# Optimization experiments

Hardware: AMD Instinct MI355X
Metric: run time of the kernel (lower is better)

The kernel has to match this reference:

```python
import jax, jax.numpy as jnp
import numpy as np

DIM = 2048
N_HEADS = 32
N_KV_HEADS = 8
HEAD_DIM = 64
REPEATS = N_HEADS // N_KV_HEADS
SLIDING_WINDOW = 1024
EPS = 1e-6
B, T = 2, 2048


def _alibi_slopes(n):
    # n_heads=32 is a power of 2
    r = 2.0 ** (-8.0 / n)
    return jnp.asarray([r ** i for i in range(n)], dtype=jnp.float32)


def _rms_norm(x, w, eps):
    # RMSNorm over the last (flattened heads*head_dim) axis
    var = jnp.mean(x * x, axis=-1, keepdims=True)
    return x * jax.lax.rsqrt(var + eps) * w


def setup_inputs() -> dict:
    key = jax.random.key(0)
    ks = jax.random.split(key, 6)
    s = 0.02
    return {
        "x": jax.random.normal(ks[0], (B, T, DIM), jnp.float32),
        "wq": jax.random.normal(ks[1], (N_HEADS * HEAD_DIM, DIM), jnp.float32) * s,
        "wk": jax.random.normal(ks[2], (N_KV_HEADS * HEAD_DIM, DIM), jnp.float32) * s,
        "wv": jax.random.normal(ks[3], (N_KV_HEADS * HEAD_DIM, DIM), jnp.float32) * s,
        "wo": jax.random.normal(ks[4], (DIM, N_HEADS * HEAD_DIM), jnp.float32) * s,
        "q_norm_w": jnp.ones((N_HEADS * HEAD_DIM,), jnp.float32),
        "k_norm_w": jnp.ones((N_KV_HEADS * HEAD_DIM,), jnp.float32),
    }


def reference(x, wq, wk, wv, wo, q_norm_w, k_norm_w):
    bsz, seqlen, _ = x.shape
    xq = _rms_norm(x @ wq.T, q_norm_w, EPS)
    xk = _rms_norm(x @ wk.T, k_norm_w, EPS)
    xv = x @ wv.T
    xq = xq.reshape(bsz, seqlen, N_HEADS, HEAD_DIM).transpose(0, 2, 1, 3)  # b h t d
    xk = xk.reshape(bsz, seqlen, N_KV_HEADS, HEAD_DIM).transpose(0, 2, 1, 3)
    xv = xv.reshape(bsz, seqlen, N_KV_HEADS, HEAD_DIM).transpose(0, 2, 1, 3)
    # GQA: repeat_interleave kv heads
    xk = jnp.repeat(xk, REPEATS, axis=1)
    xv = jnp.repeat(xv, REPEATS, axis=1)

    pos = jnp.arange(seqlen)
    dist = pos[None, :] - pos[:, None]                     # [t,s] = s - t (<=0 on causal side)
    slopes = _alibi_slopes(N_HEADS)
    alibi = slopes[:, None, None] * dist.astype(jnp.float32)  # [h,t,s]
    allowed = (dist <= 0) & (dist >= -SLIDING_WINDOW)      # causal + sliding window
    bias = jnp.where(allowed[None], alibi, -jnp.inf)       # [h,t,s]

    scale = 1.0 / jnp.sqrt(jnp.asarray(HEAD_DIM, jnp.float32))
    scores = jnp.einsum("bhtd,bhsd->bhts", xq, xk) * scale + bias[None]
    attn = jax.nn.softmax(scores, axis=-1)
    out = jnp.einsum("bhts,bhsd->bhtd", attn, xv)          # [b,h,t,d]
    out = out.transpose(0, 2, 1, 3).reshape(bsz, seqlen, N_HEADS * HEAD_DIM)
    return out @ wo.T
```

## Files before the change

kernel.cpp:

```cpp
#include <hip/hip_runtime.h>


typedef _Float16 f16;
typedef __attribute__((ext_vector_type(8))) _Float16 f16x8;
typedef __attribute__((ext_vector_type(4))) _Float16 f16x4;
typedef __attribute__((ext_vector_type(4))) float f32x4;

#define T_ 2048
#define NH 32
#define NKV 8
#define HD 64
#define WINDOW 1024
#define EPS_ 1e-6f
#define LOG2E 1.44269504088896340736f
#define LDQKV 3072

__device__ inline void async16(void* lds, const void* g) {
  __builtin_amdgcn_global_load_lds(
      (const __attribute__((address_space(1))) unsigned int*)g,
      (__attribute__((address_space(3))) unsigned int*)lds, 16, 0, 0);
}

struct CvtArgs {
  const float* src[5];
  f16* dst[5];
  int n4[5];
};
__global__ __launch_bounds__(256) void cvt_multi(CvtArgs a) {
  const int seg = blockIdx.y;
  const float* in = a.src[seg];
  f16* out = a.dst[seg];
  const int n4 = a.n4[seg];
  for (int i = blockIdx.x * blockDim.x + threadIdx.x; i < n4;
       i += gridDim.x * blockDim.x) {
    float4 v = ((const float4*)in)[i];
    f16x4 o;
    o[0] = (f16)v.x; o[1] = (f16)v.y; o[2] = (f16)v.z; o[3] = (f16)v.w;
    ((f16x4*)out)[i] = o;
  }
}

__global__ __launch_bounds__(256) void gemm_nt(const f16* __restrict__ A,
                                               const f16* __restrict__ B,
                                               void* __restrict__ C,
                                               int M, int N, int K, int ldc,
                                               int out_f32) {
  __shared__ f16 As[128 * 32];
  __shared__ f16 Bs[128 * 32];
  const int tid = threadIdx.x;
  const int lane = tid & 63, wave = tid >> 6;
  const int quad = (lane >> 4), l16 = lane & 15;
  const int wm = (wave >> 1) * 64, wn = (wave & 1) * 64;
  const int m0 = blockIdx.y * 128, n0 = blockIdx.x * 128;
  const int srow = tid >> 2, scol = (tid & 3) * 8;
  const f16* gA = A + (size_t)(m0 + srow) * K + scol;
  const f16* gB = B + (size_t)(n0 + srow) * K + scol;
  f16* lA = As + tid * 8;
  f16* lB = Bs + tid * 8;
  const size_t rowK64 = (size_t)64 * K;

  f32x4 acc[4][4] = {};

  for (int k0 = 0; k0 < K; k0 += 32) {
    async16(lA, gA + k0);
    async16(lA + 2048, gA + rowK64 + k0);
    async16(lB, gB + k0);
    async16(lB + 2048, gB + rowK64 + k0);
    __syncthreads();
    f16x8 af[4], bf[4];
#pragma unroll
    for (int i = 0; i < 4; ++i)
      af[i] = *(const f16x8*)(As + (wm + i * 16 + l16) * 32 + quad * 8);
#pragma unroll
    for (int i = 0; i < 4; ++i)
      bf[i] = *(const f16x8*)(Bs + (wn + i * 16 + l16) * 32 + quad * 8);
#pragma unroll
    for (int i = 0; i < 4; ++i)
#pragma unroll
      for (int j = 0; j < 4; ++j)
        acc[i][j] = __builtin_amdgcn_mfma_f32_16x16x32_f16(af[i], bf[j], acc[i][j], 0, 0, 0);
    __syncthreads();
  }
#pragma unroll
  for (int i = 0; i < 4; ++i) {
    const int row0 = m0 + wm + i * 16 + quad * 4;
#pragma unroll
    for (int j = 0; j < 4; ++j) {
      const int col = n0 + wn + j * 16 + l16;
#pragma unroll
      for (int r = 0; r < 4; ++r) {
        const float v = acc[i][j][r];
        if (out_f32) ((float*)C)[(size_t)(row0 + r) * ldc + col] = v;
        else         ((f16*)C)[(size_t)(row0 + r) * ldc + col] = (f16)v;
      }
    }
  }
}

__global__ __launch_bounds__(256) void rmsnorm2(f16* __restrict__ xqkv,
                                                const float* __restrict__ qw,
                                                const float* __restrict__ kw) {
  __shared__ float red[4];
  const int which = blockIdx.y;
  const int N = which ? 512 : 2048;
  const float* w = which ? kw : qw;
  f16* p = xqkv + (size_t)blockIdx.x * LDQKV + (which ? 2048 : 0);
  const int tid = threadIdx.x;
  const int per = N >> 8;
  float ss = 0.f;
#pragma unroll 4
  for (int i = 0; i < per; ++i) {
    const float v = (float)p[tid * per + i];
    ss += v * v;
  }
#pragma unroll
  for (int off = 32; off > 0; off >>= 1) ss += __shfl_down(ss, off);
  if ((tid & 63) == 0) red[tid >> 6] = ss;
  __syncthreads();
  const float scale = rsqrtf((red[0] + red[1] + red[2] + red[3]) / (float)N + EPS_);
#pragma unroll 4
  for (int i = 0; i < per; ++i) {
    const int c = tid * per + i;
    p[c] = (f16)((float)p[c] * scale * w[c]);
  }
}

__global__ __launch_bounds__(256) void vtrans(const f16* __restrict__ xqkv,
                                              f16* __restrict__ Vt) {
  __shared__ f16 L[64][72];
  const int t0 = blockIdx.x * 64;
  const int b = blockIdx.y >> 3, kh = blockIdx.y & 7;
  const int tid = threadIdx.x;
  const int r = tid >> 3, c = (tid & 7) * 8;
#pragma unroll
  for (int rp = 0; rp < 2; ++rp) {
    const int rr = r + rp * 32;
    *(f16x8*)(&L[rr][c]) =
        *(const f16x8*)(xqkv + (size_t)(b * T_ + t0 + rr) * LDQKV + 2560 + kh * 64 + c);
  }
  __syncthreads();
#pragma unroll
  for (int rp = 0; rp < 2; ++rp) {
    const int d = r + rp * 32;
    f16x8 o;
#pragma unroll
    for (int j = 0; j < 8; ++j) o[j] = L[c + j][d];
    *(f16x8*)(Vt + (size_t)((b * 8 + kh) * 64 + d) * T_ + t0 + c) = o;
  }
}

__global__ __launch_bounds__(256) void attn(const f16* __restrict__ Q,
                                            const f16* __restrict__ Kb,
                                            const f16* __restrict__ Vt_g,
                                            f16* __restrict__ O) {
  constexpr int LDW = 72;
  __shared__ f16 Qs[64 * LDW];
  __shared__ f16 Ks[64 * LDW];
  __shared__ f16 Vts[64 * LDW];
  __shared__ float Lx[4][16];

  const int qt = blockIdx.x, h = blockIdx.y, b = blockIdx.z;
  const int kh = h >> 2;
  const int q0 = qt * 64;
  const int tid = threadIdx.x;
  const int lane = tid & 63, wave = tid >> 6;
  const int quad = lane >> 4, l16 = lane & 15;
  const float scale2 = 0.125f * LOG2E;
  const float slope2 = exp2f(-0.25f * (float)h) * LOG2E;
  const float M2 = 10.0f;

  const int sr = tid >> 3, sc = (tid & 7) * 8;

#pragma unroll
  for (int rp = 0; rp < 2; ++rp) {
    const int rr = sr + rp * 32;
    *(f16x8*)(Qs + rr * LDW + sc) =
        *(const f16x8*)(Q + (size_t)(b * T_ + q0 + rr) * LDQKV + h * HD + sc);
  }
  __syncthreads();
  f16x8 qf[2];
#pragma unroll
  for (int kc = 0; kc < 2; ++kc)
    qf[kc] = *(const f16x8*)(Qs + (wave * 16 + l16) * LDW + kc * 32 + quad * 8);
  f16* Ps = Qs + wave * 16 * LDW;

  f32x4 o_acc[4] = {};
  float lsum = 0.f;

  const int kt_lo = (q0 >= WINDOW) ? ((q0 - WINDOW) >> 6) : 0;
  const int my_q = q0 + wave * 16 + l16;
  const size_t vbase = (size_t)((b * 8 + kh) * 64) * T_;

  float snbr[16];
#pragma unroll
  for (int nb = 0; nb < 4; ++nb)
#pragma unroll
    for (int r = 0; r < 4; ++r) snbr[nb * 4 + r] = slope2 * (float)(nb * 16 + r);
  float base = slope2 * (float)(kt_lo * 64 + quad * 4 - my_q) - M2;
  const float bstep = slope2 * 64.0f;

  f16x8 kreg[2], vreg[2];
  auto prefetch = [&](int k0) {
#pragma unroll
    for (int rp = 0; rp < 2; ++rp) {
      const int rr = sr + rp * 32;
      kreg[rp] = *(const f16x8*)(Kb + (size_t)(b * T_ + k0 + rr) * LDQKV + kh * HD + sc);
      vreg[rp] = *(const f16x8*)(Vt_g + vbase + (size_t)rr * T_ + k0 + sc);
    }
  };
  prefetch(kt_lo * 64);

  for (int kt = kt_lo; kt <= qt; ++kt) {
    const int k0 = kt * 64;
#pragma unroll
    for (int rp = 0; rp < 2; ++rp) {
      *(f16x8*)(Ks + (sr + rp * 32) * LDW + sc) = kreg[rp];
      *(f16x8*)(Vts + (sr + rp * 32) * LDW + sc) = vreg[rp];
    }
    __syncthreads();
    if (kt < qt) prefetch(k0 + 64);

    f32x4 s[4];
#pragma unroll
    for (int nb = 0; nb < 4; ++nb) {
      f32x4 a = {0.f, 0.f, 0.f, 0.f};
#pragma unroll
      for (int kc = 0; kc < 2; ++kc) {
        f16x8 kf = *(const f16x8*)(Ks + (nb * 16 + l16) * LDW + kc * 32 + quad * 8);
        a = __builtin_amdgcn_mfma_f32_16x16x32_f16(kf, qf[kc], a, 0, 0, 0);
      }
      s[nb] = a;
    }

    const bool maskt = (kt == qt) || (q0 + 63 - k0 > WINDOW);
#pragma unroll
    for (int nb = 0; nb < 4; ++nb) {
      f16x4 pk;
#pragma unroll
      for (int r = 0; r < 4; ++r) {
        float v = fmaf(s[nb][r], scale2, base + snbr[nb * 4 + r]);
        if (maskt) {
          const int dist = k0 + nb * 16 + quad * 4 + r - my_q;
          if (dist > 0 || dist < -WINDOW) v = -1e30f;
        }
        const float p = __builtin_amdgcn_exp2f(v);
        lsum += p;
        pk[r] = (f16)p;
      }
      *(f16x4*)(Ps + l16 * LDW + nb * 16 + quad * 4) = pk;
    }
    base += bstep;

#pragma unroll
    for (int nb = 0; nb < 4; ++nb) {
#pragma unroll
      for (int kc = 0; kc < 2; ++kc) {
        f16x8 pa = *(const f16x8*)(Ps + l16 * LDW + kc * 32 + quad * 8);
        f16x8 vb = *(const f16x8*)(Vts + (nb * 16 + l16) * LDW + kc * 32 + quad * 8);
        o_acc[nb] = __builtin_amdgcn_mfma_f32_16x16x32_f16(pa, vb, o_acc[nb], 0, 0, 0);
      }
    }
    __syncthreads();
  }

  lsum += __shfl_xor(lsum, 16);
  lsum += __shfl_xor(lsum, 32);
  if (quad == 0) Lx[wave][l16] = lsum;
  float rl[4];
#pragma unroll
  for (int r = 0; r < 4; ++r) rl[r] = 1.0f / Lx[wave][quad * 4 + r];

#pragma unroll
  for (int r = 0; r < 4; ++r) {
    const int q = q0 + wave * 16 + quad * 4 + r;
#pragma unroll
    for (int nb = 0; nb < 4; ++nb)
      O[(size_t)(b * T_ + q) * (NH * HD) + h * HD + nb * 16 + l16] =
          (f16)(o_acc[nb][r] * rl[r]);
  }
}

extern "C" void kernel_launch(void* const* d_in, const int* in_sizes, int n_in,
                              void* d_out, int out_size, void* d_ws, size_t ws_size,
                              hipStream_t stream) {
  const float* x  = (const float*)d_in[0];
  const float* wq = (const float*)d_in[1];
  const float* wk = (const float*)d_in[2];
  const float* wv = (const float*)d_in[3];
  const float* wo = (const float*)d_in[4];
  const float* qw = (const float*)d_in[5];
  const float* kw = (const float*)d_in[6];
  float* out = (float*)d_out;

  char* ws = (char*)d_ws;
  size_t off = 0;
  auto carve = [&](size_t bytes) -> char* {
    char* p = ws + off;
    off += (bytes + 255) & ~(size_t)255;
    return p;
  };
  f16* xh    = (f16*)carve((size_t)4096 * 2048 * 2);
  f16* wqkvh = (f16*)carve((size_t)3072 * 2048 * 2);
  f16* woh   = (f16*)carve((size_t)2048 * 2048 * 2);
  f16* xqkv  = (f16*)carve((size_t)4096 * 3072 * 2);
  f16* Vt = wqkvh + (size_t)2048 * 2048;
  f16* ao = xh;

  CvtArgs ca;
  ca.src[0] = x;  ca.dst[0] = xh;                            ca.n4[0] = (4096 * 2048) / 4;
  ca.src[1] = wq; ca.dst[1] = wqkvh;                         ca.n4[1] = (2048 * 2048) / 4;
  ca.src[2] = wk; ca.dst[2] = wqkvh + (size_t)2048 * 2048;   ca.n4[2] = (512 * 2048) / 4;
  ca.src[3] = wv; ca.dst[3] = wqkvh + (size_t)2560 * 2048;   ca.n4[3] = (512 * 2048) / 4;
  ca.src[4] = wo; ca.dst[4] = woh;                           ca.n4[4] = (2048 * 2048) / 4;
  cvt_multi<<<dim3(1024, 5), 256, 0, stream>>>(ca);

  gemm_nt<<<dim3(24, 32), 256, 0, stream>>>(xh, wqkvh, xqkv, 4096, 3072, 2048, LDQKV, 0);
  rmsnorm2<<<dim3(4096, 2), 256, 0, stream>>>(xqkv, qw, kw);
  vtrans<<<dim3(32, 16), 256, 0, stream>>>(xqkv, Vt);
  attn<<<dim3(32, 32, 2), 256, 0, stream>>>(xqkv, xqkv + 2048, Vt, ao);
  gemm_nt<<<dim3(16, 32), 256, 0, stream>>>(ao, woh, out, 4096, 2048, 2048, 2048, 1);
}
```

Before: 330.8 us.

## Replace GEMM with 256x256 double-buffered, swizzled-LDS 8-wave kernel

Replaces the 128x128, single-buffered, 4-wave GEMM with a 256x256 tile, 8-wave kernel. It uses K=64 steps, double-buffered LDS filled by async global-to-LDS loads, XOR-swizzled LDS addressing to avoid bank conflicts, and an XCD-aware block remap. Global loads for the next tile are interleaved with MFMA phases, and s_setprio raises priority during the MFMA phases. This is meant to raise arithmetic intensity and hide load latency in both projection GEMMs. In exchange it needs 128KB of dynamic LDS, which limits occupancy, and launches only 192 and 128 workgroups, which may underfill the GPU.

New measurement: 326.6 us. Within noise of the previous version (-1.3%).

```diff
diff --git a/kernel.cpp b/kernel.cpp
--- a/kernel.cpp
+++ b/kernel.cpp
@@ -40,56 +40,141 @@
   }
 }
 
-__global__ __launch_bounds__(256) void gemm_nt(const f16* __restrict__ A,
-                                               const f16* __restrict__ B,
-                                               void* __restrict__ C,
-                                               int M, int N, int K, int ldc,
-                                               int out_f32) {
-  __shared__ f16 As[128 * 32];
-  __shared__ f16 Bs[128 * 32];
+
+#define DSRD(p, off) (*(const f16x8*)((p) + (off)))
+
+#define LOADA(mh)                                                             \
+  {                                                                           \
+    _Pragma("unroll") for (int i = 0; i < 4; ++i) {                           \
+      af[i][0] = DSRD(cA, bufo + abase + (mh) * 8192 + i * 2048 + xk0);       \
+      af[i][1] = DSRD(cA, bufo + abase + (mh) * 8192 + i * 2048 + xk1);       \
+    }                                                                         \
+  }
+
+#define LOADB(bfv, nh)                                                        \
+  {                                                                           \
+    _Pragma("unroll") for (int j = 0; j < 2; ++j) {                           \
+      bfv[j][0] = DSRD(cB, bufo + bbase + (nh) * 4096 + j * 2048 + xk0);      \
+      bfv[j][1] = DSRD(cB, bufo + bbase + (nh) * 4096 + j * 2048 + xk1);      \
+    }                                                                         \
+  }
+
+#define FENCE_MFMA(mh, nh, bfv)                                               \
+  {                                                                           \
+    __builtin_amdgcn_s_barrier();                                             \
+    asm volatile("s_waitcnt lgkmcnt(0)" ::: "memory");                        \
+    __builtin_amdgcn_sched_barrier(0);                                        \
+    __builtin_amdgcn_s_setprio(1);                                            \
+    _Pragma("unroll") for (int i = 0; i < 4; ++i) {                           \
+      _Pragma("unroll") for (int j = 0; j < 2; ++j) {                         \
+        acc[(mh) * 4 + i][(nh) * 2 + j] =                                     \
+            __builtin_amdgcn_mfma_f32_16x16x32_f16(                           \
+                af[i][0], bfv[j][0], acc[(mh) * 4 + i][(nh) * 2 + j], 0, 0, 0); \
+        acc[(mh) * 4 + i][(nh) * 2 + j] =                                     \
+            __builtin_amdgcn_mfma_f32_16x16x32_f16(                           \
+                af[i][1], bfv[j][1], acc[(mh) * 4 + i][(nh) * 2 + j], 0, 0, 0); \
+      }                                                                       \
+    }                                                                         \
+    __builtin_amdgcn_s_setprio(0);                                            \
+  }
+
+__global__ __launch_bounds__(512, 2) void gemm_nt8(const f16* __restrict__ A,
+                                                   const f16* __restrict__ B,
+                                                   void* __restrict__ C,
+                                                   int M, int N, int K, int ldc,
+                                                   int out_f32) {
+  extern __shared__ char smem[];
+  f16* sA = (f16*)smem;
+  f16* sB = (f16*)(smem + 65536);
+
+  const int gx = gridDim.x;
+  const int nwg = gx * gridDim.y;
+  int bid = blockIdx.y * gx + blockIdx.x;
+  if (!(nwg & 7)) bid = (bid & 7) * (nwg >> 3) + (bid >> 3);
+  const int m0 = (bid / gx) * 256;
+  const int n0 = (bid % gx) * 256;
+
   const int tid = threadIdx.x;
-  const int lane = tid & 63, wave = tid >> 6;
-  const int quad = (lane >> 4), l16 = lane & 15;
-  const int wm = (wave >> 1) * 64, wn = (wave & 1) * 64;
-  const int m0 = blockIdx.y * 128, n0 = blockIdx.x * 128;
-  const int srow = tid >> 2, scol = (tid & 3) * 8;
-  const f16* gA = A + (size_t)(m0 + srow) * K + scol;
-  const f16* gB = B + (size_t)(n0 + srow) * K + scol;
-  f16* lA = As + tid * 8;
-  f16* lB = Bs + tid * 8;
-  const size_t rowK64 = (size_t)64 * K;
-
-  f32x4 acc[4][4] = {};
-
-  for (int k0 = 0; k0 < K; k0 += 32) {
-    async16(lA, gA + k0);
-    async16(lA + 2048, gA + rowK64 + k0);
-    async16(lB, gB + k0);
-    async16(lB + 2048, gB + rowK64 + k0);
-    __syncthreads();
-    f16x8 af[4], bf[4];
-#pragma unroll
-    for (int i = 0; i < 4; ++i)
-      af[i] = *(const f16x8*)(As + (wm + i * 16 + l16) * 32 + quad * 8);
-#pragma unroll
-    for (int i = 0; i < 4; ++i)
-      bf[i] = *(const f16x8*)(Bs + (wn + i * 16 + l16) * 32 + quad * 8);
-#pragma unroll
-    for (int i = 0; i < 4; ++i)
-#pragma unroll
-      for (int j = 0; j < 4; ++j)
-        acc[i][j] = __builtin_amdgcn_mfma_f32_16x16x32_f16(af[i], bf[j], acc[i][j], 0, 0, 0);
-    __syncthreads();
-  }
-#pragma unroll
-  for (int i = 0; i < 4; ++i) {
-    const int row0 = m0 + wm + i * 16 + quad * 4;
-#pragma unroll
-    for (int j = 0; j < 4; ++j) {
-      const int col = n0 + wn + j * 16 + l16;
+  const int lane = tid & 63;
+  const int wave = tid >> 6;
+  const int quad = lane >> 4, l16 = lane & 15;
+  const int wm = wave >> 2, wn = wave & 3;
+
+  const int srow = tid >> 3;
+  const int sgr = (((tid & 7) ^ (srow & 7))) * 8;
+  const f16* gA = A + (size_t)(m0 + srow) * K + sgr;
+  const f16* gB = B + (size_t)(n0 + srow) * K + sgr;
+  const size_t r64 = (size_t)64 * K;
+
+  const char* cA = (const char*)sA;
+  const char* cB = (const char*)sB;
+  const int xm = (l16 & 7) << 4;
+  const int xk0 = (quad * 16) ^ xm;
+  const int xk1 = (64 + quad * 16) ^ xm;
+  const int abase = (wm * 128 + l16) * 128;
+  const int bbase = (wn * 64 + l16) * 128;
+
+  f32x4 acc[8][4] = {};
+  const int nt = K >> 6;
+
+#pragma unroll
+  for (int a = 0; a < 4; ++a) {
+    async16(sA + a * 4096 + tid * 8, gA + (size_t)a * r64);
+    async16(sB + a * 4096 + tid * 8, gB + (size_t)a * r64);
+  }
+  asm volatile("s_waitcnt vmcnt(0)" ::: "memory");
+  __builtin_amdgcn_s_barrier();
+
+  for (int t = 0; t < nt; ++t) {
+    const int bufo = (t & 1) << 15;
+    f16* sAn = sA + ((t & 1) ^ 1) * 16384;
+    f16* sBn = sB + ((t & 1) ^ 1) * 16384;
+    const bool st = (t + 1 < nt);
+    const size_t gk = (size_t)(t + 1) * 64;
+
+    f16x8 af[4][2], bf0[2][2], bf1[2][2];
+
+    LOADA(0);
+    LOADB(bf0, 0);
+    if (st) {
+      async16(sAn + 0 * 4096 + tid * 8, gA + 0 * r64 + gk);
+      async16(sAn + 1 * 4096 + tid * 8, gA + 1 * r64 + gk);
+      async16(sBn + 0 * 4096 + tid * 8, gB + 0 * r64 + gk);
+      async16(sBn + 1 * 4096 + tid * 8, gB + 1 * r64 + gk);
+    }
+    FENCE_MFMA(0, 0, bf0);
+    __builtin_amdgcn_s_barrier();
+
+    LOADB(bf1, 1);
+    if (st) {
+      async16(sAn + 2 * 4096 + tid * 8, gA + 2 * r64 + gk);
+      async16(sAn + 3 * 4096 + tid * 8, gA + 3 * r64 + gk);
+      async16(sBn + 2 * 4096 + tid * 8, gB + 2 * r64 + gk);
+      async16(sBn + 3 * 4096 + tid * 8, gB + 3 * r64 + gk);
+    }
+    FENCE_MFMA(0, 1, bf1);
+    __builtin_amdgcn_s_barrier();
+
+    LOADA(1);
+    LOADB(bf0, 0);
+    FENCE_MFMA(1, 0, bf0);
+    __builtin_amdgcn_s_barrier();
+
+    LOADB(bf1, 1);
+    FENCE_MFMA(1, 1, bf1);
+    if (st) asm volatile("s_waitcnt vmcnt(0)" ::: "memory");
+    __builtin_amdgcn_s_barrier();
+  }
+
+#pragma unroll
+  for (int im = 0; im < 8; ++im) {
+    const int row0 = m0 + wm * 128 + im * 16 + quad * 4;
+#pragma unroll
+    for (int jn = 0; jn < 4; ++jn) {
+      const int col = n0 + wn * 64 + jn * 16 + l16;
 #pragma unroll
       for (int r = 0; r < 4; ++r) {
-        const float v = acc[i][j][r];
+        const float v = acc[im][jn][r];
         if (out_f32) ((float*)C)[(size_t)(row0 + r) * ldc + col] = v;
         else         ((f16*)C)[(size_t)(row0 + r) * ldc + col] = (f16)v;
       }
@@ -306,6 +391,14 @@
   f16* Vt = wqkvh + (size_t)2048 * 2048;
   f16* ao = xh;
 
+  static bool attr_done = false;
+  if (!attr_done) {
+    (void)hipFuncSetAttribute((const void*)gemm_nt8,
+                              hipFuncAttributeMaxDynamicSharedMemorySize,
+                              131072);
+    attr_done = true;
+  }
+
   CvtArgs ca;
   ca.src[0] = x;  ca.dst[0] = xh;                            ca.n4[0] = (4096 * 2048) / 4;
   ca.src[1] = wq; ca.dst[1] = wqkvh;                         ca.n4[1] = (2048 * 2048) / 4;
@@ -314,9 +407,9 @@
   ca.src[4] = wo; ca.dst[4] = woh;                           ca.n4[4] = (2048 * 2048) / 4;
   cvt_multi<<<dim3(1024, 5), 256, 0, stream>>>(ca);
 
-  gemm_nt<<<dim3(24, 32), 256, 0, stream>>>(xh, wqkvh, xqkv, 4096, 3072, 2048, LDQKV, 0);
+  gemm_nt8<<<dim3(12, 16), 512, 131072, stream>>>(xh, wqkvh, xqkv, 4096, 3072, 2048, LDQKV, 0);
   rmsnorm2<<<dim3(4096, 2), 256, 0, stream>>>(xqkv, qw, kw);
   vtrans<<<dim3(32, 16), 256, 0, stream>>>(xqkv, Vt);
   attn<<<dim3(32, 32, 2), 256, 0, stream>>>(xqkv, xqkv + 2048, Vt, ao);
-  gemm_nt<<<dim3(16, 32), 256, 0, stream>>>(ao, woh, out, 4096, 2048, 2048, 2048, 1);
-}
+  gemm_nt8<<<dim3(8, 16), 512, 131072, stream>>>(ao, woh, out, 4096, 2048, 2048, 2048, 1);
+}
```
